# Optimization experiments

Hardware: AMD Instinct MI355X
Metric: run time of the kernel (lower is better)

The kernel has to match this reference:

```python
import jax, jax.numpy as jnp
import numpy as np

S, B, LAG, H, F = 10, 16384, 5, 512, 5

def setup_inputs() -> dict:
    key = jax.random.key(0)
    ks = jax.random.split(key, 16)
    sc = 0.05
    inp = {
        'x': jax.random.normal(ks[0], (S, B, LAG), jnp.float32),
        'W_in': jax.random.normal(ks[1], (H, LAG), jnp.float32) * sc,
        'b_in': jax.random.normal(ks[2], (H,), jnp.float32) * sc,
        'Wih0': jax.random.normal(ks[3], (4 * H, H), jnp.float32) * sc,
        'Whh0': jax.random.normal(ks[4], (4 * H, H), jnp.float32) * sc,
        'bih0': jax.random.normal(ks[5], (4 * H,), jnp.float32) * sc,
        'bhh0': jax.random.normal(ks[6], (4 * H,), jnp.float32) * sc,
        'Wih1': jax.random.normal(ks[7], (4 * H, H), jnp.float32) * sc,
        'Whh1': jax.random.normal(ks[8], (4 * H, H), jnp.float32) * sc,
        'bih1': jax.random.normal(ks[9], (4 * H,), jnp.float32) * sc,
        'bhh1': jax.random.normal(ks[10], (4 * H,), jnp.float32) * sc,
        'W_out': jax.random.normal(ks[11], (1, H), jnp.float32) * sc,
        'b_out': jax.random.normal(ks[12], (1,), jnp.float32) * sc,
        'W_f': jax.random.normal(ks[13], (F, H), jnp.float32) * sc,
        'b_f': jax.random.normal(ks[14], (F,), jnp.float32) * sc,
    }
    return inp

def _lstm_cell(g, h, c, Whh, bhh):
    # g: precomputed input-side gates [B,4H]; add recurrent part, PyTorch gate order i,f,g,o
    g = g + h @ Whh.T + bhh
    i, f, gg, o = jnp.split(g, 4, axis=-1)
    c_new = jax.nn.sigmoid(f) * c + jax.nn.sigmoid(i) * jnp.tanh(gg)
    h_new = jax.nn.sigmoid(o) * jnp.tanh(c_new)
    return h_new, c_new

def reference(x, W_in, b_in, Wih0, Whh0, bih0, bhh0, Wih1, Whh1, bih1, bhh1, W_out, b_out, W_f, b_f):
    # input projection for all steps at once: [S,B,H]
    u = x @ W_in.T + b_in
    # precompute input-side LSTM gates for layer 0: [S,B,4H]
    g0_all = u @ Wih0.T + bih0
    zeros = jnp.zeros((B, H), x.dtype)

    def step(carry, g0_t):
        h0, c0, h1, c1 = carry
        h0, c0 = _lstm_cell(g0_t, h0, c0, Whh0, bhh0)
        g1 = h0 @ Wih1.T + bih1  # dropout between layers is eval-mode no-op
        h1, c1 = _lstm_cell(g1, h1, c1, Whh1, bhh1)
        return (h0, c0, h1, c1), h1

    (h0, c0, h1, c1), hs = jax.lax.scan(step, (zeros, zeros, zeros, zeros), g0_all)
    # per-step scalar outputs: [S,B,1] -> [B,S]
    step_out = (hs @ W_out.T + b_out)[:, :, 0].T
    # forecast head from last layer's final hidden state: [B,F]
    fc = h1 @ W_f.T + b_f
    outputs = jnp.concatenate([step_out, fc], axis=1)  # [B, S+F]
    h_n = jnp.stack([h0, h1])  # [2,B,H]
    c_n = jnp.stack([c0, c1])
    return outputs, h_n, c_n
```

## Files before the change

kernel.cpp:

```cpp
#include <hip/hip_runtime.h>
#include <hip/hip_bf16.h>

constexpr int S   = 10;
constexpr int Bsz = 16384;
constexpr int LAG = 5;
constexpr int H   = 512;
constexpr int G4  = 4 * H;
constexpr int F   = 5;
constexpr int BH  = Bsz * H;
constexpr int OUT_HN = Bsz * (S + F);
constexpr int OUT_CN = OUT_HN + 2 * BH;

typedef __attribute__((ext_vector_type(8))) short short8;
typedef __attribute__((ext_vector_type(4))) float f32x4;

__device__ __forceinline__ float sigf(float x) { return 1.0f / (1.0f + __expf(-x)); }
__device__ __forceinline__ float tanh_fast(float x) {
    float e = __expf(2.0f * x);
    return 1.0f - 2.0f / (e + 1.0f);
}

__device__ __forceinline__ void gload_lds16(const void* g, void* l) {
    __builtin_amdgcn_global_load_lds(
        (const __attribute__((address_space(1))) unsigned int*)g,
        (__attribute__((address_space(3))) unsigned int*)l, 16, 0, 0);
}

__global__ __launch_bounds__(256)
void prep_kernel(const float* __restrict__ W_in,  const float* __restrict__ b_in,
                 const float* __restrict__ Wih0,  const float* __restrict__ Whh0,
                 const float* __restrict__ bih0,  const float* __restrict__ bhh0,
                 const float* __restrict__ Wih1,  const float* __restrict__ Whh1,
                 const float* __restrict__ bih1,  const float* __restrict__ bhh1,
                 __hip_bfloat16* __restrict__ W0b, __hip_bfloat16* __restrict__ W1b,
                 float* __restrict__ A0r, float* __restrict__ b0r,
                 float* __restrict__ b1r)
{
    const int r   = blockIdx.x;
    const int tid = threadIdx.x;

    for (int k = tid; k < H; k += 256)
        W0b[r * H + k] = __float2bfloat16(Whh0[r * H + k]);
    for (int k = tid; k < 2 * H; k += 256)
        W1b[r * 2 * H + k] = __float2bfloat16(
            (k < H) ? Wih1[r * H + k] : Whh1[r * H + (k - H)]);

    if (tid < LAG) {
        float s = 0.f;
        for (int h = 0; h < H; ++h) s += Wih0[r * H + h] * W_in[h * LAG + tid];
        A0r[r * LAG + tid] = s;
    } else if (tid == 5) {
        float s = 0.f;
        for (int h = 0; h < H; ++h) s += Wih0[r * H + h] * b_in[h];
        b0r[r] = s + bih0[r] + bhh0[r];
    } else if (tid == 6) {
        b1r[r] = bih1[r] + bhh1[r];
    }
}

__global__ __launch_bounds__(256)
void lstm_gemm(const __hip_bfloat16* __restrict__ Aseg0,
               const __hip_bfloat16* __restrict__ Aseg1,
               int nseg,
               const __hip_bfloat16* __restrict__ W, int ldw,
               const float* __restrict__ bias,
               const float* __restrict__ xs,
               const float* __restrict__ A0r,
               const float* __restrict__ c_in,
               float* __restrict__ c_out,
               float* __restrict__ h32_out,
               __hip_bfloat16* __restrict__ hb16_out,
               int hcol)
{
    __shared__ __align__(16) short As[128 * 64];
    __shared__ __align__(16) short Bs[128 * 64];
    __shared__ float xls[128 * LAG];
    __shared__ float a0ls[128 * LAG];

    const int tid  = threadIdx.x;
    const int lane = tid & 63;
    const int quad = lane >> 4;
    const int li   = lane & 15;
    const int ww   = tid >> 6;
    const int wy   = ww >> 1;
    const int wx   = ww & 1;

    const int bM = blockIdx.y * 128;
    const int cn = blockIdx.x * 32;

    const bool has_x = (xs != nullptr);
    if (has_x) {
        for (int i = tid; i < 128 * LAG; i += 256) {
            const int row = i / LAG, l = i % LAG;
            xls[i] = xs[(size_t)(bM + row) * LAG + l];
        }
        for (int i = tid; i < 128 * LAG; i += 256) {
            const int cl = i / LAG, l = i % LAG;
            const int r  = (cl >> 5) * H + cn + (cl & 31);
            a0ls[i] = A0r[r * LAG + l];
        }
    }
    __syncthreads();

    f32x4 acc[4][4];
    #pragma unroll
    for (int i = 0; i < 4; ++i)
        #pragma unroll
        for (int j = 0; j < 4; ++j) acc[i][j] = (f32x4){0.f, 0.f, 0.f, 0.f};

    size_t a_off[4], w_off[4];
    #pragma unroll
    for (int r = 0; r < 4; ++r) {
        const int idx  = r * 256 + tid;
        const int row  = idx >> 3;
        const int kcg  = ((idx & 7) ^ (row & 7)) * 8;
        a_off[r] = (size_t)(bM + row) * 1024 + kcg;
        const int rr = (row >> 5) * H + cn + (row & 31);
        w_off[r] = (size_t)rr * ldw + kcg;
    }

    for (int seg = 0; seg < nseg; ++seg) {
        const __hip_bfloat16* Abuf = seg ? Aseg1 : Aseg0;
        const __hip_bfloat16* pa[4];
        const __hip_bfloat16* pw[4];
        #pragma unroll
        for (int r = 0; r < 4; ++r) {
            pa[r] = Abuf + a_off[r] + seg * 512;
            pw[r] = W    + w_off[r] + seg * 512;
        }
        for (int t = 0; t < 8; ++t) {
            __syncthreads();
            #pragma unroll
            for (int r = 0; r < 4; ++r)
                gload_lds16(pa[r], &As[(r * 256 + tid) * 8]);
            #pragma unroll
            for (int r = 0; r < 4; ++r)
                gload_lds16(pw[r], &Bs[(r * 256 + tid) * 8]);
            #pragma unroll
            for (int r = 0; r < 4; ++r) { pa[r] += 64; pw[r] += 64; }
            __syncthreads();

            #pragma unroll
            for (int c = 0; c < 2; ++c) {
                short8 af[4], bf[4];
                #pragma unroll
                for (int mt = 0; mt < 4; ++mt) {
                    const int row = wy * 64 + mt * 16 + li;
                    const int kch = (c * 4 + quad) ^ (row & 7);
                    af[mt] = *(const short8*)&As[row * 64 + kch * 8];
                }
                #pragma unroll
                for (int g = 0; g < 4; ++g) {
                    const int cl  = g * 32 + wx * 16 + li;
                    const int kch = (c * 4 + quad) ^ (cl & 7);
                    bf[g] = *(const short8*)&Bs[cl * 64 + kch * 8];
                }
                #pragma unroll
                for (int mt = 0; mt < 4; ++mt)
                    #pragma unroll
                    for (int g = 0; g < 4; ++g)
                        acc[mt][g] = __builtin_amdgcn_mfma_f32_16x16x32_bf16(
                            af[mt], bf[g], acc[mt][g], 0, 0, 0);
            }
        }
    }

    const int n = cn + wx * 16 + li;
    float bias4[4], a0reg[4][LAG];
    #pragma unroll
    for (int g = 0; g < 4; ++g) bias4[g] = bias[g * H + n];
    if (has_x) {
        #pragma unroll
        for (int g = 0; g < 4; ++g)
            #pragma unroll
            for (int l = 0; l < LAG; ++l)
                a0reg[g][l] = a0ls[(g * 32 + wx * 16 + li) * LAG + l];
    }

    #pragma unroll
    for (int mt = 0; mt < 4; ++mt) {
        #pragma unroll
        for (int reg = 0; reg < 4; ++reg) {
            const int b_loc = wy * 64 + mt * 16 + quad * 4 + reg;
            const int b     = bM + b_loc;
            float g4[4];
            #pragma unroll
            for (int g = 0; g < 4; ++g) g4[g] = acc[mt][g][reg] + bias4[g];
            if (has_x) {
                #pragma unroll
                for (int l = 0; l < LAG; ++l) {
                    const float xv = xls[b_loc * LAG + l];
                    #pragma unroll
                    for (int g = 0; g < 4; ++g) g4[g] = fmaf(xv, a0reg[g][l], g4[g]);
                }
            }
            const float ig = sigf(g4[0]);
            const float fg = sigf(g4[1]);
            const float gg = tanh_fast(g4[2]);
            const float og = sigf(g4[3]);
            const float cold = c_in ? c_in[(size_t)b * H + n] : 0.f;
            const float cnew = fg * cold + ig * gg;
            const float hh   = og * tanh_fast(cnew);
            c_out[(size_t)b * H + n] = cnew;
            if (h32_out) h32_out[(size_t)b * H + n] = hh;
            hb16_out[(size_t)b * 1024 + hcol + n] = __float2bfloat16(hh);
        }
    }
}

__global__ __launch_bounds__(256)
void out_head(const __hip_bfloat16* __restrict__ hcat,
              const float* __restrict__ W_out, const float* __restrict__ b_out,
              const float* __restrict__ W_f,   const float* __restrict__ b_f,
              float* __restrict__ out, int s, int last)
{
    const int wave = threadIdx.x >> 6;
    const int lane = threadIdx.x & 63;
    const int b    = blockIdx.x * 4 + wave;

    const __hip_bfloat16* hrow = hcat + (size_t)b * 1024 + 512;
    short8 hv = *(const short8*)&hrow[lane * 8];
    float h8[8];
    #pragma unroll
    for (int i = 0; i < 8; ++i) {
        union { unsigned int u; float f; } cv;
        cv.u = ((unsigned int)(unsigned short)hv[i]) << 16;
        h8[i] = cv.f;
    }

    {
        const float4 w0 = *reinterpret_cast<const float4*>(&W_out[lane * 8]);
        const float4 w1 = *reinterpret_cast<const float4*>(&W_out[lane * 8 + 4]);
        const float w8[8] = {w0.x, w0.y, w0.z, w0.w, w1.x, w1.y, w1.z, w1.w};
        float v = 0.f;
        #pragma unroll
        for (int i = 0; i < 8; ++i) v = fmaf(h8[i], w8[i], v);
        #pragma unroll
        for (int off = 32; off > 0; off >>= 1) v += __shfl_down(v, off, 64);
        if (lane == 0) out[b * (S + F) + s] = v + b_out[0];
    }
    if (last) {
        for (int f = 0; f < F; ++f) {
            const float4 w0 = *reinterpret_cast<const float4*>(&W_f[f * H + lane * 8]);
            const float4 w1 = *reinterpret_cast<const float4*>(&W_f[f * H + lane * 8 + 4]);
            const float w8[8] = {w0.x, w0.y, w0.z, w0.w, w1.x, w1.y, w1.z, w1.w};
            float v = 0.f;
            #pragma unroll
            for (int i = 0; i < 8; ++i) v = fmaf(h8[i], w8[i], v);
            #pragma unroll
            for (int off = 32; off > 0; off >>= 1) v += __shfl_down(v, off, 64);
            if (lane == 0) out[b * (S + F) + S + f] = v + b_f[f];
        }
    }
}

extern "C" void kernel_launch(void* const* d_in, const int* in_sizes, int n_in,
                              void* d_out, int out_size, void* d_ws, size_t ws_size,
                              hipStream_t stream)
{
    const float* x     = (const float*)d_in[0];
    const float* W_in  = (const float*)d_in[1];
    const float* b_in  = (const float*)d_in[2];
    const float* Wih0  = (const float*)d_in[3];
    const float* Whh0  = (const float*)d_in[4];
    const float* bih0  = (const float*)d_in[5];
    const float* bhh0  = (const float*)d_in[6];
    const float* Wih1  = (const float*)d_in[7];
    const float* Whh1  = (const float*)d_in[8];
    const float* bih1  = (const float*)d_in[9];
    const float* bhh1  = (const float*)d_in[10];
    const float* W_out = (const float*)d_in[11];
    const float* b_out = (const float*)d_in[12];
    const float* W_f   = (const float*)d_in[13];
    const float* b_f   = (const float*)d_in[14];

    float* out = (float*)d_out;
    char*  ws  = (char*)d_ws;

    __hip_bfloat16* hcat0 = (__hip_bfloat16*)ws;
    __hip_bfloat16* hcat1 = hcat0 + (size_t)Bsz * 1024;
    __hip_bfloat16* W0b   = hcat1 + (size_t)Bsz * 1024;
    __hip_bfloat16* W1b   = W0b + (size_t)G4 * H;
    float* A0r = (float*)(W1b + (size_t)G4 * 2 * H);
    float* b0r = A0r + G4 * LAG;
    float* b1r = b0r + G4;

    float* hn0 = out + OUT_HN;
    float* hn1 = out + OUT_HN + BH;
    float* c0  = out + OUT_CN;
    float* c1  = out + OUT_CN + BH;

    prep_kernel<<<dim3(G4), dim3(256), 0, stream>>>(
        W_in, b_in, Wih0, Whh0, bih0, bhh0, Wih1, Whh1, bih1, bhh1,
        W0b, W1b, A0r, b0r, b1r);

    __hip_bfloat16* hbuf[2] = {hcat0, hcat1};
    const dim3 grid(H / 32, Bsz / 128);
    const dim3 blk(256);

    for (int s = 0; s < S; ++s) {
        const bool first = (s == 0);
        const bool last  = (s == S - 1);
        __hip_bfloat16* cur  = hbuf[s & 1];
        __hip_bfloat16* prev = hbuf[(s + 1) & 1];

        lstm_gemm<<<grid, blk, 0, stream>>>(
            prev, nullptr, first ? 0 : 1, W0b, H, b0r,
            x + (size_t)s * Bsz * LAG, A0r,
            first ? nullptr : c0, c0, last ? hn0 : nullptr, cur, 0);

        lstm_gemm<<<grid, blk, 0, stream>>>(
            cur, prev, first ? 1 : 2, W1b, 2 * H, b1r,
            nullptr, nullptr,
            first ? nullptr : c1, c1, last ? hn1 : nullptr, cur, H);

        out_head<<<dim3(Bsz / 4), blk, 0, stream>>>(
            cur, W_out, b_out, W_f, b_f, out, s, last ? 1 : 0);
    }
}
```

Measured before the change: 1.711 ms.

## Triple-buffer LDS tiles, enlarge GEMM block to 256 rows, swizzle block order

The LSTM gate GEMM moves to 512-thread blocks covering 256 batch rows, so each loaded weight tile is reused across twice as many rows. LDS is triple-buffered, with global-to-LDS loads issued two tiles ahead and a manual vmcnt wait plus barrier, replacing the two full syncs per K step. The block index is remapped so neighbouring blocks share weight columns for better L2 reuse, and MFMA issue priority is raised. The risks are higher LDS use, which limits occupancy, and a hand-coded wait count that must match the number of outstanding loads.

Result: slower. 2.031 ms (+18.7%).

```diff
diff --git a/kernel.cpp b/kernel.cpp
--- a/kernel.cpp
+++ b/kernel.cpp
@@ -10,6 +10,14 @@
 constexpr int BH  = Bsz * H;
 constexpr int OUT_HN = Bsz * (S + F);
 constexpr int OUT_CN = OUT_HN + 2 * BH;
+
+constexpr int BM   = 256;
+constexpr int UN   = 32;
+constexpr int BN   = 4 * UN;
+constexpr int BK   = 64;
+constexpr int NBUF = 3;
+constexpr int A_TILE = BM * BK;
+constexpr int B_TILE = BN * BK;
 
 typedef __attribute__((ext_vector_type(8))) short short8;
 typedef __attribute__((ext_vector_type(4))) float f32x4;
@@ -58,7 +66,7 @@
     }
 }
 
-__global__ __launch_bounds__(256)
+__global__ __launch_bounds__(512, 2)
 void lstm_gemm(const __hip_bfloat16* __restrict__ Aseg0,
                const __hip_bfloat16* __restrict__ Aseg1,
                int nseg,
@@ -72,32 +80,36 @@
                __hip_bfloat16* __restrict__ hb16_out,
                int hcol)
 {
-    __shared__ __align__(16) short As[128 * 64];
-    __shared__ __align__(16) short Bs[128 * 64];
-    __shared__ float xls[128 * LAG];
-    __shared__ float a0ls[128 * LAG];
+    __shared__ __align__(16) short As[NBUF * A_TILE];
+    __shared__ __align__(16) short Bs[NBUF * B_TILE];
+    __shared__ float xls[BM * LAG];
+    __shared__ float a0ls[BN * LAG];
 
     const int tid  = threadIdx.x;
     const int lane = tid & 63;
     const int quad = lane >> 4;
     const int li   = lane & 15;
-    const int ww   = tid >> 6;
-    const int wy   = ww >> 1;
-    const int wx   = ww & 1;
-
-    const int bM = blockIdx.y * 128;
-    const int cn = blockIdx.x * 32;
+    const int wv   = tid >> 6;
+    const int wy   = wv >> 1;
+    const int wx   = wv & 1;
+
+    const int l  = blockIdx.y * gridDim.x + blockIdx.x;
+    const int v  = (l & 7) * 128 + (l >> 3);
+    const int by = v >> 4;
+    const int bx = v & 15;
+    const int bM_ = by * BM;
+    const int cn  = bx * UN;
 
     const bool has_x = (xs != nullptr);
     if (has_x) {
-        for (int i = tid; i < 128 * LAG; i += 256) {
-            const int row = i / LAG, l = i % LAG;
-            xls[i] = xs[(size_t)(bM + row) * LAG + l];
-        }
-        for (int i = tid; i < 128 * LAG; i += 256) {
-            const int cl = i / LAG, l = i % LAG;
+        for (int i = tid; i < BM * LAG; i += 512) {
+            const int row = i / LAG, ll = i % LAG;
+            xls[i] = xs[(size_t)(bM_ + row) * LAG + ll];
+        }
+        for (int i = tid; i < BN * LAG; i += 512) {
+            const int cl = i / LAG, ll = i % LAG;
             const int r  = (cl >> 5) * H + cn + (cl & 31);
-            a0ls[i] = A0r[r * LAG + l];
+            a0ls[i] = A0r[r * LAG + ll];
         }
     }
     __syncthreads();
@@ -108,61 +120,74 @@
         #pragma unroll
         for (int j = 0; j < 4; ++j) acc[i][j] = (f32x4){0.f, 0.f, 0.f, 0.f};
 
-    size_t a_off[4], w_off[4];
+    int aoff[4], woff[2];
     #pragma unroll
     for (int r = 0; r < 4; ++r) {
-        const int idx  = r * 256 + tid;
-        const int row  = idx >> 3;
-        const int kcg  = ((idx & 7) ^ (row & 7)) * 8;
-        a_off[r] = (size_t)(bM + row) * 1024 + kcg;
-        const int rr = (row >> 5) * H + cn + (row & 31);
-        w_off[r] = (size_t)rr * ldw + kcg;
-    }
-
-    for (int seg = 0; seg < nseg; ++seg) {
-        const __hip_bfloat16* Abuf = seg ? Aseg1 : Aseg0;
-        const __hip_bfloat16* pa[4];
-        const __hip_bfloat16* pw[4];
-        #pragma unroll
-        for (int r = 0; r < 4; ++r) {
-            pa[r] = Abuf + a_off[r] + seg * 512;
-            pw[r] = W    + w_off[r] + seg * 512;
-        }
-        for (int t = 0; t < 8; ++t) {
-            __syncthreads();
-            #pragma unroll
-            for (int r = 0; r < 4; ++r)
-                gload_lds16(pa[r], &As[(r * 256 + tid) * 8]);
-            #pragma unroll
-            for (int r = 0; r < 4; ++r)
-                gload_lds16(pw[r], &Bs[(r * 256 + tid) * 8]);
-            #pragma unroll
-            for (int r = 0; r < 4; ++r) { pa[r] += 64; pw[r] += 64; }
-            __syncthreads();
-
-            #pragma unroll
-            for (int c = 0; c < 2; ++c) {
-                short8 af[4], bf[4];
+        const int idx = r * 512 + tid;
+        const int row = idx >> 3;
+        const int j   = idx & 7;
+        aoff[r] = (bM_ + row) * 1024 + ((j ^ (row & 7)) * 8);
+    }
+    #pragma unroll
+    for (int r = 0; r < 2; ++r) {
+        const int idx = r * 512 + tid;
+        const int row = idx >> 3;
+        const int j   = idx & 7;
+        const int rr  = (row >> 5) * H + cn + (row & 31);
+        woff[r] = rr * ldw + ((j ^ (row & 7)) * 8);
+    }
+
+    const int NT = nseg * 8;
+
+    auto stage_tile = [&](int t) {
+        const int seg = t >> 3;
+        const int kof = seg * 512 + (t & 7) * BK;
+        const short* pa = (const short*)(seg ? Aseg1 : Aseg0) + kof;
+        const short* pw = (const short*)W + kof;
+        short* as = As + (t % NBUF) * A_TILE;
+        short* bs = Bs + (t % NBUF) * B_TILE;
+        #pragma unroll
+        for (int r = 0; r < 4; ++r)
+            gload_lds16(pa + aoff[r], &as[(r * 512 + tid) * 8]);
+        #pragma unroll
+        for (int r = 0; r < 2; ++r)
+            gload_lds16(pw + woff[r], &bs[(r * 512 + tid) * 8]);
+    };
+
+    auto compute_tile = [&](int t) {
+        const short* as = As + (t % NBUF) * A_TILE;
+        const short* bs = Bs + (t % NBUF) * B_TILE;
+        #pragma unroll
+        for (int c = 0; c < 2; ++c) {
+            const int p = (c * 4 + quad) ^ (li & 7);
+            short8 af[4], bf[4];
+            #pragma unroll
+            for (int m = 0; m < 4; ++m)
+                af[m] = *(const short8*)&as[(wy * 64 + m * 16 + li) * 64 + p * 8];
+            #pragma unroll
+            for (int g = 0; g < 4; ++g)
+                bf[g] = *(const short8*)&bs[(g * 32 + wx * 16 + li) * 64 + p * 8];
+            __builtin_amdgcn_s_setprio(1);
+            #pragma unroll
+            for (int m = 0; m < 4; ++m)
                 #pragma unroll
-                for (int mt = 0; mt < 4; ++mt) {
-                    const int row = wy * 64 + mt * 16 + li;
-                    const int kch = (c * 4 + quad) ^ (row & 7);
-                    af[mt] = *(const short8*)&As[row * 64 + kch * 8];
-                }
-                #pragma unroll
-                for (int g = 0; g < 4; ++g) {
-                    const int cl  = g * 32 + wx * 16 + li;
-                    const int kch = (c * 4 + quad) ^ (cl & 7);
-                    bf[g] = *(const short8*)&Bs[cl * 64 + kch * 8];
-                }
-                #pragma unroll
-                for (int mt = 0; mt < 4; ++mt)
-                    #pragma unroll
-                    for (int g = 0; g < 4; ++g)
-                        acc[mt][g] = __builtin_amdgcn_mfma_f32_16x16x32_bf16(
-                            af[mt], bf[g], acc[mt][g], 0, 0, 0);
-            }
-        }
+                for (int g = 0; g < 4; ++g)
+                    acc[m][g] = __builtin_amdgcn_mfma_f32_16x16x32_bf16(
+                        af[m], bf[g], acc[m][g], 0, 0, 0);
+            __builtin_amdgcn_s_setprio(0);
+        }
+    };
+
+    if (NT) {
+        stage_tile(0);
+        stage_tile(1);
+        for (int t = 0; t < NT - 1; ++t) {
+            asm volatile("s_waitcnt vmcnt(6)\n\ts_barrier" ::: "memory");
+            if (t + 2 < NT) stage_tile(t + 2);
+            compute_tile(t);
+        }
+        asm volatile("s_waitcnt vmcnt(0)\n\ts_barrier" ::: "memory");
+        compute_tile(NT - 1);
     }
 
     const int n = cn + wx * 16 + li;
@@ -173,8 +198,8 @@
         #pragma unroll
         for (int g = 0; g < 4; ++g)
             #pragma unroll
-            for (int l = 0; l < LAG; ++l)
-                a0reg[g][l] = a0ls[(g * 32 + wx * 16 + li) * LAG + l];
+            for (int ll = 0; ll < LAG; ++ll)
+                a0reg[g][ll] = a0ls[(g * 32 + wx * 16 + li) * LAG + ll];
     }
 
     #pragma unroll
@@ -182,16 +207,16 @@
         #pragma unroll
         for (int reg = 0; reg < 4; ++reg) {
             const int b_loc = wy * 64 + mt * 16 + quad * 4 + reg;
-            const int b     = bM + b_loc;
+            const int b     = bM_ + b_loc;
             float g4[4];
             #pragma unroll
             for (int g = 0; g < 4; ++g) g4[g] = acc[mt][g][reg] + bias4[g];
             if (has_x) {
                 #pragma unroll
-                for (int l = 0; l < LAG; ++l) {
-                    const float xv = xls[b_loc * LAG + l];
+                for (int ll = 0; ll < LAG; ++ll) {
+                    const float xv = xls[b_loc * LAG + ll];
                     #pragma unroll
-                    for (int g = 0; g < 4; ++g) g4[g] = fmaf(xv, a0reg[g][l], g4[g]);
+                    for (int g = 0; g < 4; ++g) g4[g] = fmaf(xv, a0reg[g][ll], g4[g]);
                 }
             }
             const float ig = sigf(g4[0]);
@@ -295,8 +320,8 @@
         W0b, W1b, A0r, b0r, b1r);
 
     __hip_bfloat16* hbuf[2] = {hcat0, hcat1};
-    const dim3 grid(H / 32, Bsz / 128);
-    const dim3 blk(256);
+    const dim3 grid(H / UN, Bsz / BM);
+    const dim3 blk(512);
 
     for (int s = 0; s < S; ++s) {
         const bool first = (s == 0);
@@ -314,7 +339,7 @@
             nullptr, nullptr,
             first ? nullptr : c1, c1, last ? hn1 : nullptr, cur, H);
 
-        out_head<<<dim3(Bsz / 4), blk, 0, stream>>>(
+        out_head<<<dim3(Bsz / 4), dim3(256), 0, stream>>>(
             cur, W_out, b_out, W_f, b_f, out, s, last ? 1 : 0);
     }
 }
```
